# Optimization experiments

Hardware: AMD Instinct MI355X
Metric: run time of the kernel (lower is better)

The kernel has to match this reference:

```python
import jax, jax.numpy as jnp
import numpy as np

ATT_HEAD = 12
IN_DIM = 768
OUT_DIM = IN_DIM // ATT_HEAD
LEAKY_ALPHA = 0.2
B, N = 8, 512


def setup_inputs() -> dict:
    key = jax.random.key(0)
    ks = jax.random.split(key, 8)
    feat_in = jax.random.normal(ks[0], (B, N, IN_DIM), dtype=jnp.float32)
    adj = jax.random.randint(ks[1], (B, N, N), 0, 2) > 0
    # xavier_uniform for W: fan_in=in_dim, fan_out=out_dim
    lim_W = float(np.sqrt(6.0 / (IN_DIM + OUT_DIM)))
    W = jax.random.uniform(ks[2], (ATT_HEAD, IN_DIM, OUT_DIM), minval=-lim_W, maxval=lim_W, dtype=jnp.float32)
    b = jnp.zeros((OUT_DIM,), dtype=jnp.float32)
    lim_w = float(np.sqrt(6.0 / (OUT_DIM + 1)))
    w_src = jax.random.uniform(ks[3], (ATT_HEAD, OUT_DIM, 1), minval=-lim_w, maxval=lim_w, dtype=jnp.float32)
    w_dst = jax.random.uniform(ks[4], (ATT_HEAD, OUT_DIM, 1), minval=-lim_w, maxval=lim_w, dtype=jnp.float32)
    # xavier_normal for H.weight [in_dim, in_dim]
    std_H = float(np.sqrt(2.0 / (IN_DIM + IN_DIM)))
    H_w = jax.random.normal(ks[5], (IN_DIM, IN_DIM), dtype=jnp.float32) * std_H
    H_b = jax.random.normal(ks[6], (IN_DIM,), dtype=jnp.float32) * 0.01
    return {"feat_in": feat_in, "adj": adj, "W": W, "b": b,
            "w_src": w_src, "w_dst": w_dst, "H_w": H_w, "H_b": H_b}


def reference(feat_in, adj, W, b, w_src, w_dst, H_w, H_b):
    # h: [B, heads, N, out_dim]
    h = jnp.einsum('bnd,ade->bane', feat_in, W)
    th = jnp.tanh(h)
    attn_src = jnp.einsum('bane,aeo->bano', th, w_src)  # [B,A,N,1]
    attn_dst = jnp.einsum('bane,aeo->bano', th, w_dst)  # [B,A,N,1]
    attn = attn_src + jnp.swapaxes(attn_dst, 2, 3)      # [B,A,N,N]
    attn = jnp.where(attn >= 0, attn, LEAKY_ALPHA * attn)
    mask = ~adj[:, None, :, :]                           # [B,1,N,N]
    attn = jnp.where(mask, jnp.float32(-999.0), attn)
    attn = jax.nn.softmax(attn, axis=-1)
    feat_out = jnp.einsum('banm,bame->bane', attn, h) + b
    feat_out = jnp.swapaxes(feat_out, 1, 2).reshape(feat_in.shape[0], feat_in.shape[1], -1)
    feat_out = jax.nn.elu(feat_out)
    gate = jax.nn.sigmoid(feat_in @ H_w.T + H_b)
    return gate * feat_out + (1.0 - gate) * feat_in
```

## Files before the change

kernel.cpp:

```cpp
#include <hip/hip_runtime.h>
#include <hip/hip_bf16.h>

#define BB 8
#define NN 512
#define AH 12
#define DIN 768
#define EE 64
#define MM (BB*NN)
#define YY (BB*AH)
#define LEAKY 0.2f

typedef unsigned short u16;
typedef unsigned int u32;
typedef __attribute__((ext_vector_type(8))) short short8;
typedef __attribute__((ext_vector_type(4))) float f32x4;
typedef __attribute__((ext_vector_type(4))) u32 u32x4;

static __device__ __forceinline__ u16 f2bf(float f) {
    u32 u = __builtin_bit_cast(u32, f);
    u32 r = (u + 0x7FFFu + ((u >> 16) & 1u)) >> 16;
    return (u16)r;
}
static __device__ __forceinline__ u32 pk2(float a, float b) {
    return (u32)f2bf(a) | ((u32)f2bf(b) << 16);
}
static __device__ __forceinline__ u32 pk2t(float a, float b) {
    return (__builtin_bit_cast(u32, a) >> 16) | (__builtin_bit_cast(u32, b) & 0xFFFF0000u);
}
static __device__ __forceinline__ float ftanh(float x) {
    x = fminf(fmaxf(x, -15.f), 15.f);
    return 1.f - 2.f / (__expf(2.f * x) + 1.f);
}
static __device__ __forceinline__ float sigm(float z) {
    z = fminf(fmaxf(z, -80.f), 80.f);
    return 1.f / (1.f + __expf(-z));
}
static __device__ __forceinline__ void gl_lds16(const u16* g, u16* l) {
    __builtin_amdgcn_global_load_lds((const __attribute__((address_space(1))) unsigned int*)g,
                                     (__attribute__((address_space(3))) unsigned int*)l,
                                     16, 0, 0);
}

static __device__ __forceinline__ void mfma_probe(int lane, int* prow, int* pcol) {
    int q = lane >> 4, x = lane & 15;
    short8 af, bf;
#pragma unroll
    for (int j = 0; j < 8; j++) {
        int k = q * 8 + j;
        af[j] = (short)f2bf((k < 16) ? (float)(x * 16 + k) : 0.f);
        bf[j] = (short)f2bf((k == x) ? 1.f : 0.f);
    }
    f32x4 d = {};
    d = __builtin_amdgcn_mfma_f32_16x16x32_bf16(af, bf, d, 0, 0, 0);
#pragma unroll
    for (int r = 0; r < 4; r++) {
        int v = (int)(d[r] + 0.5f);
        prow[r] = v >> 4;
        pcol[r] = v & 15;
    }
}

#define N_FEAT (MM*DIN)
#define N_W    (AH*DIN*EE)
#define PACK_BLOCKS (MM/4)
#define CONV_BLOCKS ((N_FEAT + 2*N_W)/256)
__global__ __launch_bounds__(256) void prep_kernel(const int* __restrict__ adj,
                                                   const float* __restrict__ feat,
                                                   const float* __restrict__ W,
                                                   const float* __restrict__ Hw,
                                                   u32* __restrict__ maskbuf,
                                                   u16* __restrict__ featb,
                                                   u16* __restrict__ Wt,
                                                   u16* __restrict__ Hwb) {
    int blk = blockIdx.x, t = threadIdx.x;
    if (blk < PACK_BLOCKS) {
        int w = t >> 6, ln = t & 63;
        int row = blk * 4 + w;
        const int* ar = adj + (size_t)row * NN;
#pragma unroll
        for (int it = 0; it < 8; it++) {
            unsigned long long bal = __ballot(ar[it * 64 + ln] != 0);
            if (ln == 0) {
                maskbuf[row * 16 + it * 2]     = (u32)bal;
                maskbuf[row * 16 + it * 2 + 1] = (u32)(bal >> 32);
            }
        }
        return;
    }
    int i = (blk - PACK_BLOCKS) * 256 + t;
    if (i < N_FEAT) { featb[i] = f2bf(feat[i]); return; }
    int i2 = i - N_FEAT;
    if (i2 < N_W) {
        int a = i2 / (DIN * EE), rem = i2 % (DIN * EE);
        int e = rem / DIN, d = rem % DIN;
        Wt[i2] = f2bf(W[a * (DIN * EE) + d * EE + e]);
        return;
    }
    int i3 = i2 - N_W;
    Hwb[i3] = f2bf(Hw[i3]);
}

__global__ __launch_bounds__(256) void gemm_fused_kernel(const u16* __restrict__ featb,
                                                         const u16* __restrict__ Wt,
                                                         const u16* __restrict__ Hwb,
                                                         const float* __restrict__ wsrc,
                                                         const float* __restrict__ wdst,
                                                         const float* __restrict__ Hb,
                                                         u16* __restrict__ hT,
                                                         float2* __restrict__ Spair,
                                                         float2* __restrict__ Dpair,
                                                         float* __restrict__ Gbuf) {
    __shared__ u16 As[64 * 64];
    __shared__ u16 BsW[64 * 64];
    __shared__ u16 BsG[64 * 64];
    __shared__ alignas(16) float cs[64][68];
    int t = threadIdx.x, w = t >> 6, lane = t & 63, q = lane >> 4, x = lane & 15;
    int m0 = blockIdx.x * 64, a = blockIdx.y;

    int wm = w & 1, wn = w >> 1, xr = x & 7;
    int srow = t >> 3;
    int skoff = ((t & 7) ^ (srow & 7)) * 8;
    const u16* Agp  = featb + (size_t)m0 * DIN + srow * DIN + skoff;
    const u16* BWgp = Wt + (size_t)a * EE * DIN + srow * DIN + skoff;
    const u16* BGgp = Hwb + (size_t)(a * EE) * DIN + srow * DIN + skoff;
    u16* Asw  = As  + w * 512;
    u16* BWsw = BsW + w * 512;
    u16* BGsw = BsG + w * 512;
    const u16* ApA  = As  + (wm * 32 + x) * 64;
    const u16* ApBW = BsW + (wn * 32 + x) * 64;
    const u16* ApBG = BsG + (wn * 32 + x) * 64;
    f32x4 aW00 = {}, aW01 = {}, aW10 = {}, aW11 = {};
    f32x4 aG00 = {}, aG01 = {}, aG10 = {}, aG11 = {};

    for (int k0 = 0; k0 < DIN; k0 += 64) {
        gl_lds16(Agp + k0, Asw);
        gl_lds16(Agp + 32 * DIN + k0, Asw + 2048);
        gl_lds16(BWgp + k0, BWsw);
        gl_lds16(BWgp + 32 * DIN + k0, BWsw + 2048);
        gl_lds16(BGgp + k0, BGsw);
        gl_lds16(BGgp + 32 * DIN + k0, BGsw + 2048);
        __syncthreads();
#pragma unroll
        for (int kk = 0; kk < 2; kk++) {
            int c8 = ((q + kk * 4) ^ xr) * 8;
            short8 a0 = *(const short8*)(ApA + c8);
            short8 a1 = *(const short8*)(ApA + 16 * 64 + c8);
            short8 bW0 = *(const short8*)(ApBW + c8);
            short8 bW1 = *(const short8*)(ApBW + 16 * 64 + c8);
            short8 bG0 = *(const short8*)(ApBG + c8);
            short8 bG1 = *(const short8*)(ApBG + 16 * 64 + c8);
            aW00 = __builtin_amdgcn_mfma_f32_16x16x32_bf16(a0, bW0, aW00, 0, 0, 0);
            aW01 = __builtin_amdgcn_mfma_f32_16x16x32_bf16(a0, bW1, aW01, 0, 0, 0);
            aW10 = __builtin_amdgcn_mfma_f32_16x16x32_bf16(a1, bW0, aW10, 0, 0, 0);
            aW11 = __builtin_amdgcn_mfma_f32_16x16x32_bf16(a1, bW1, aW11, 0, 0, 0);
            aG00 = __builtin_amdgcn_mfma_f32_16x16x32_bf16(a0, bG0, aG00, 0, 0, 0);
            aG01 = __builtin_amdgcn_mfma_f32_16x16x32_bf16(a0, bG1, aG01, 0, 0, 0);
            aG10 = __builtin_amdgcn_mfma_f32_16x16x32_bf16(a1, bG0, aG10, 0, 0, 0);
            aG11 = __builtin_amdgcn_mfma_f32_16x16x32_bf16(a1, bG1, aG11, 0, 0, 0);
        }
        __syncthreads();
    }

    int prow[4], pcol[4];
    mfma_probe(lane, prow, pcol);

#pragma unroll
    for (int r = 0; r < 4; r++) {
        cs[wm * 32 + prow[r]][wn * 32 + pcol[r]]           = aW00[r];
        cs[wm * 32 + prow[r]][wn * 32 + 16 + pcol[r]]      = aW01[r];
        cs[wm * 32 + 16 + prow[r]][wn * 32 + pcol[r]]      = aW10[r];
        cs[wm * 32 + 16 + prow[r]][wn * 32 + 16 + pcol[r]] = aW11[r];
    }
    __syncthreads();

    int b = m0 >> 9;
    int y = b * AH + a;
    int nbase = m0 & 511;
    {
        int kcb = nbase >> 3;
#pragma unroll
        for (int i = 0; i < 2; i++) {
            int idx = i * 256 + t;
            int kcl = idx >> 6, e = idx & 63;
            int r0 = kcl * 8;
            u32x4 wv = { pk2(cs[r0 + 0][e], cs[r0 + 1][e]),
                         pk2(cs[r0 + 2][e], cs[r0 + 3][e]),
                         pk2(cs[r0 + 4][e], cs[r0 + 5][e]),
                         pk2(cs[r0 + 6][e], cs[r0 + 7][e]) };
            *(u32x4*)&hT[((((size_t)y << 6) + kcb + kcl) << 6 | e) * 8] = wv;
        }
    }
    {
        int r = t >> 2, cg = t & 3;
        float s = 0.f, d = 0.f;
#pragma unroll
        for (int i = 0; i < 16; i++) {
            int e2 = cg * 16 + i;
            float th = ftanh(cs[r][e2]);
            s += th * wsrc[a * EE + e2];
            d += th * wdst[a * EE + e2];
        }
        s += __shfl_xor(s, 1); s += __shfl_xor(s, 2);
        d += __shfl_xor(d, 1); d += __shfl_xor(d, 2);
        if (cg == 0) {
            s = fminf(fmaxf(s, -40.f), 40.f);
            d = fminf(fmaxf(d, -40.f), 40.f);
            Spair[y * NN + nbase + r] = make_float2(__expf(s), __expf(0.2f * s));
            Dpair[y * NN + nbase + r] = make_float2(__expf(d), __expf(0.2f * d));
        }
    }
    __syncthreads();

#pragma unroll
    for (int r = 0; r < 4; r++) {
        cs[wm * 32 + prow[r]][wn * 32 + pcol[r]]           = aG00[r];
        cs[wm * 32 + prow[r]][wn * 32 + 16 + pcol[r]]      = aG01[r];
        cs[wm * 32 + 16 + prow[r]][wn * 32 + pcol[r]]      = aG10[r];
        cs[wm * 32 + 16 + prow[r]][wn * 32 + 16 + pcol[r]] = aG11[r];
    }
    __syncthreads();

    {
        int n0 = a * EE;
        float4 hb = *(const float4*)&Hb[n0 + (t & 15) * 4];
#pragma unroll
        for (int p = 0; p < 4; p++) {
            int ml = p * 16 + (t >> 4), c4 = (t & 15) * 4;
            float4 v4 = *(const float4*)&cs[ml][c4];
            size_t idx = (size_t)(m0 + ml) * DIN + n0 + c4;
            float4 o;
            o.x = sigm(v4.x + hb.x);
            o.y = sigm(v4.y + hb.y);
            o.z = sigm(v4.z + hb.z);
            o.w = sigm(v4.w + hb.w);
            *(float4*)&Gbuf[idx] = o;
        }
    }
}

__global__ __launch_bounds__(256) void attn_kernel(const u16* __restrict__ hT,
                                                   const float2* __restrict__ Spair,
                                                   const float2* __restrict__ Dpair,
                                                   const u32* __restrict__ maskbuf,
                                                   const float* __restrict__ bias,
                                                   const float* __restrict__ Gbuf,
                                                   const float* __restrict__ feat,
                                                   float* __restrict__ out) {
    __shared__ alignas(16) float2 sd2[NN];
    __shared__ u32 smask[64][17];
    __shared__ float silv[64];
    __shared__ alignas(16) float cs[64][68];

    int t = threadIdx.x;
    int y = blockIdx.y, bb = y / AH, a = y % AH;
    int i0 = blockIdx.x * 64;
    int w = t >> 6, lane = t & 63, q = lane >> 4, x = lane & 15;

    sd2[t] = Dpair[y * NN + t];
    sd2[t + 256] = Dpair[y * NN + 256 + t];
#pragma unroll
    for (int p = 0; p < 4; p++) {
        int idx = p * 256 + t, r = idx >> 4, c = idx & 15;
        smask[r][c] = maskbuf[((bb << 9) + i0 + r) * 16 + c];
    }
    __syncthreads();

    int rowl = w * 16 + x;
    float2 se = Spair[y * NN + i0 + rowl];
    float es1 = se.x, es2 = se.y;

    u32 anym = 0;
#pragma unroll
    for (int c = 0; c < 16; c++) anym |= smask[rowl][c];
    int uni = (anym == 0);

    const u16* hTy = hT + ((size_t)y << 12) * 8;
    f32x4 acc[4] = {};
    float lsum = 0.f;

#pragma unroll 2
    for (int k0 = 0; k0 < NN; k0 += 32) {
        u32 mb = smask[rowl][k0 >> 5] >> (q * 8);
        float pv[8];
#pragma unroll
        for (int j = 0; j < 8; j++) {
            float2 dp = sd2[k0 + q * 8 + j];
            float m1 = es1 * dp.x;
            float m2 = es2 * dp.y;
            float p = (m1 >= 1.f) ? m1 : m2;
            p = ((mb >> j) & 1) ? p : 0.f;
            p = uni ? 1.0f : p;
            lsum += p;
            pv[j] = p;
        }
        short8 af = __builtin_bit_cast(short8, (u32x4){
            pk2t(pv[0], pv[1]), pk2t(pv[2], pv[3]),
            pk2t(pv[4], pv[5]), pk2t(pv[6], pv[7])});
        const u16* hp = hTy + ((((k0 >> 3) + q) << 6) + x) * 8;
        short8 b0 = *(const short8*)(hp);
        short8 b1 = *(const short8*)(hp + 16 * 8);
        short8 b2 = *(const short8*)(hp + 32 * 8);
        short8 b3 = *(const short8*)(hp + 48 * 8);
        acc[0] = __builtin_amdgcn_mfma_f32_16x16x32_bf16(af, b0, acc[0], 0, 0, 0);
        acc[1] = __builtin_amdgcn_mfma_f32_16x16x32_bf16(af, b1, acc[1], 0, 0, 0);
        acc[2] = __builtin_amdgcn_mfma_f32_16x16x32_bf16(af, b2, acc[2], 0, 0, 0);
        acc[3] = __builtin_amdgcn_mfma_f32_16x16x32_bf16(af, b3, acc[3], 0, 0, 0);
    }

    lsum += __shfl_xor(lsum, 16);
    lsum += __shfl_xor(lsum, 32);
    if (q == 0) silv[rowl] = 1.f / fmaxf(lsum, 1e-30f);

    int prow[4], pcol[4];
    mfma_probe(lane, prow, pcol);
#pragma unroll
    for (int nt = 0; nt < 4; nt++)
#pragma unroll
        for (int r = 0; r < 4; r++)
            cs[w * 16 + prow[r]][nt * 16 + pcol[r]] = acc[nt][r];
    __syncthreads();

    float4 b4 = *(const float4*)&bias[(t & 15) * 4];
#pragma unroll
    for (int p = 0; p < 4; p++) {
        int nl = p * 16 + (t >> 4), e4 = (t & 15) * 4;
        float il = silv[nl];
        float4 c4 = *(const float4*)&cs[nl][e4];
        size_t base = ((size_t)(bb << 9) + i0 + nl) * DIN + a * EE + e4;
        float4 g4 = *(const float4*)&Gbuf[base];
        float4 f4 = *(const float4*)&feat[base];
        float4 o;
        float v, e;
        v = c4.x * il + b4.x; e = v > 0.f ? v : __expf(v) - 1.f; o.x = g4.x * e + (1.f - g4.x) * f4.x;
        v = c4.y * il + b4.y; e = v > 0.f ? v : __expf(v) - 1.f; o.y = g4.y * e + (1.f - g4.y) * f4.y;
        v = c4.z * il + b4.z; e = v > 0.f ? v : __expf(v) - 1.f; o.z = g4.z * e + (1.f - g4.z) * f4.z;
        v = c4.w * il + b4.w; e = v > 0.f ? v : __expf(v) - 1.f; o.w = g4.w * e + (1.f - g4.w) * f4.w;
        *(float4*)&out[base] = o;
    }
}

extern "C" void kernel_launch(void* const* d_in, const int* in_sizes, int n_in,
                              void* d_out, int out_size, void* d_ws, size_t ws_size,
                              hipStream_t stream) {
    const float* feat  = (const float*)d_in[0];
    const int*   adj   = (const int*)  d_in[1];
    const float* W     = (const float*)d_in[2];
    const float* bvec  = (const float*)d_in[3];
    const float* wsrc  = (const float*)d_in[4];
    const float* wdst  = (const float*)d_in[5];
    const float* Hw    = (const float*)d_in[6];
    const float* Hb    = (const float*)d_in[7];
    float* out = (float*)d_out;

    char* ws = (char*)d_ws;
    u16*    featb   = (u16*)(ws);
    u16*    Wt      = (u16*)(ws + 6291456);
    u16*    Hwb     = (u16*)(ws + 7471104);
    u16*    hT      = (u16*)(ws + 8650752);
    float2* Spair   = (float2*)(ws + 14942208);
    float2* Dpair   = (float2*)(ws + 15335424);
    u32*    maskbuf = (u32*)(ws + 15728640);
    float*  Gbuf    = (float*)(ws + 15990784);

    prep_kernel<<<PACK_BLOCKS + CONV_BLOCKS, 256, 0, stream>>>(
        adj, feat, W, Hw, maskbuf, featb, Wt, Hwb);
    gemm_fused_kernel<<<dim3(MM / 64, AH), 256, 0, stream>>>(
        featb, Wt, Hwb, wsrc, wdst, Hb, hT, Spair, Dpair, Gbuf);
    attn_kernel<<<dim3(NN / 64, YY), 256, 0, stream>>>(
        hT, Spair, Dpair, maskbuf, bvec, Gbuf, feat, out);
}
```

Baseline: 122.4 us.

## Vectorize prep conversions, tile W transpose via LDS, streamline attention prob packing

The prep kernel now converts feat and H_w to bf16 four elements per thread with float4 loads, and transposes W through a shared-memory tile so both reads and writes are coalesced. Previously each of those elements was handled by its own thread, and the W transpose did strided global reads. In the attention loop, pairs of float2 loads become float4 loads, the compare-select becomes fmaxf, and truncating bf16 packing is replaced by the hardware v_cvt_pk_bf16_f32 instruction. That instruction rounds where the old code truncated, so the numerics shift slightly. Swapping the select for fmaxf assumes the two stored exponent products relate the way the original condition did.

Result: no change. 120.9 us (-1.3%).

```diff
diff --git a/kernel.cpp b/kernel.cpp
--- a/kernel.cpp
+++ b/kernel.cpp
@@ -15,6 +15,7 @@
 typedef __attribute__((ext_vector_type(8))) short short8;
 typedef __attribute__((ext_vector_type(4))) float f32x4;
 typedef __attribute__((ext_vector_type(4))) u32 u32x4;
+typedef __attribute__((ext_vector_type(4))) u16 u16x4;
 
 static __device__ __forceinline__ u16 f2bf(float f) {
     u32 u = __builtin_bit_cast(u32, f);
@@ -24,8 +25,10 @@
 static __device__ __forceinline__ u32 pk2(float a, float b) {
     return (u32)f2bf(a) | ((u32)f2bf(b) << 16);
 }
-static __device__ __forceinline__ u32 pk2t(float a, float b) {
-    return (__builtin_bit_cast(u32, a) >> 16) | (__builtin_bit_cast(u32, b) & 0xFFFF0000u);
+static __device__ __forceinline__ u32 cvtpk(float a, float b) {
+    u32 r;
+    asm("v_cvt_pk_bf16_f32 %0, %1, %2" : "=v"(r) : "v"(a), "v"(b));
+    return r;
 }
 static __device__ __forceinline__ float ftanh(float x) {
     x = fminf(fmaxf(x, -15.f), 15.f);
@@ -63,7 +66,11 @@
 #define N_FEAT (MM*DIN)
 #define N_W    (AH*DIN*EE)
 #define PACK_BLOCKS (MM/4)
-#define CONV_BLOCKS ((N_FEAT + 2*N_W)/256)
+#define FEATV_BLOCKS (N_FEAT/1024)
+#define HWBV_BLOCKS (N_W/1024)
+#define WT_BLOCKS (AH*(DIN/64))
+#define PREP_BLOCKS (PACK_BLOCKS + FEATV_BLOCKS + HWBV_BLOCKS + WT_BLOCKS)
+
 __global__ __launch_bounds__(256) void prep_kernel(const int* __restrict__ adj,
                                                    const float* __restrict__ feat,
                                                    const float* __restrict__ W,
@@ -87,17 +94,43 @@
         }
         return;
     }
-    int i = (blk - PACK_BLOCKS) * 256 + t;
-    if (i < N_FEAT) { featb[i] = f2bf(feat[i]); return; }
-    int i2 = i - N_FEAT;
-    if (i2 < N_W) {
-        int a = i2 / (DIN * EE), rem = i2 % (DIN * EE);
-        int e = rem / DIN, d = rem % DIN;
-        Wt[i2] = f2bf(W[a * (DIN * EE) + d * EE + e]);
+    blk -= PACK_BLOCKS;
+    if (blk < FEATV_BLOCKS) {
+        int i = blk * 1024 + t * 4;
+        float4 v = *(const float4*)&feat[i];
+        u16x4 o = { f2bf(v.x), f2bf(v.y), f2bf(v.z), f2bf(v.w) };
+        *(u16x4*)&featb[i] = o;
         return;
     }
-    int i3 = i2 - N_W;
-    Hwb[i3] = f2bf(Hw[i3]);
+    blk -= FEATV_BLOCKS;
+    if (blk < HWBV_BLOCKS) {
+        int i = blk * 1024 + t * 4;
+        float4 v = *(const float4*)&Hw[i];
+        u16x4 o = { f2bf(v.x), f2bf(v.y), f2bf(v.z), f2bf(v.w) };
+        *(u16x4*)&Hwb[i] = o;
+        return;
+    }
+    blk -= HWBV_BLOCKS;
+    __shared__ float tile[64][65];
+    int a = blk / (DIN / 64), d0 = (blk % (DIN / 64)) * 64;
+    int rl = t >> 4, c4 = (t & 15) * 4;
+#pragma unroll
+    for (int i = 0; i < 4; i++) {
+        int dl = i * 16 + rl;
+        float4 v = *(const float4*)&W[((size_t)a * DIN + d0 + dl) * EE + c4];
+        tile[dl][c4 + 0] = v.x;
+        tile[dl][c4 + 1] = v.y;
+        tile[dl][c4 + 2] = v.z;
+        tile[dl][c4 + 3] = v.w;
+    }
+    __syncthreads();
+#pragma unroll
+    for (int i = 0; i < 4; i++) {
+        int e = i * 16 + rl;
+        u16x4 o = { f2bf(tile[c4 + 0][e]), f2bf(tile[c4 + 1][e]),
+                    f2bf(tile[c4 + 2][e]), f2bf(tile[c4 + 3][e]) };
+        *(u16x4*)&Wt[(size_t)a * EE * DIN + (size_t)e * DIN + d0 + c4] = o;
+    }
 }
 
 __global__ __launch_bounds__(256) void gemm_fused_kernel(const u16* __restrict__ featb,
@@ -281,21 +314,24 @@
 #pragma unroll 2
     for (int k0 = 0; k0 < NN; k0 += 32) {
         u32 mb = smask[rowl][k0 >> 5] >> (q * 8);
+        const float4* sdp = (const float4*)&sd2[k0 + q * 8];
         float pv[8];
 #pragma unroll
-        for (int j = 0; j < 8; j++) {
-            float2 dp = sd2[k0 + q * 8 + j];
-            float m1 = es1 * dp.x;
-            float m2 = es2 * dp.y;
-            float p = (m1 >= 1.f) ? m1 : m2;
-            p = ((mb >> j) & 1) ? p : 0.f;
-            p = uni ? 1.0f : p;
-            lsum += p;
-            pv[j] = p;
+        for (int jj = 0; jj < 4; jj++) {
+            float4 d4 = sdp[jj];
+            float p0 = fmaxf(es1 * d4.x, es2 * d4.y);
+            float p1 = fmaxf(es1 * d4.z, es2 * d4.w);
+            p0 = ((mb >> (2 * jj)) & 1) ? p0 : 0.f;
+            p1 = ((mb >> (2 * jj + 1)) & 1) ? p1 : 0.f;
+            p0 = uni ? 1.0f : p0;
+            p1 = uni ? 1.0f : p1;
+            lsum += p0 + p1;
+            pv[2 * jj] = p0;
+            pv[2 * jj + 1] = p1;
         }
         short8 af = __builtin_bit_cast(short8, (u32x4){
-            pk2t(pv[0], pv[1]), pk2t(pv[2], pv[3]),
-            pk2t(pv[4], pv[5]), pk2t(pv[6], pv[7])});
+            cvtpk(pv[0], pv[1]), cvtpk(pv[2], pv[3]),
+            cvtpk(pv[4], pv[5]), cvtpk(pv[6], pv[7])});
         const u16* hp = hTy + ((((k0 >> 3) + q) << 6) + x) * 8;
         short8 b0 = *(const short8*)(hp);
         short8 b1 = *(const short8*)(hp + 16 * 8);
@@ -362,7 +398,7 @@
     u32*    maskbuf = (u32*)(ws + 15728640);
     float*  Gbuf    = (float*)(ws + 15990784);
 
-    prep_kernel<<<PACK_BLOCKS + CONV_BLOCKS, 256, 0, stream>>>(
+    prep_kernel<<<PREP_BLOCKS, 256, 0, stream>>>(
         adj, feat, W, Hw, maskbuf, featb, Wt, Hwb);
     gemm_fused_kernel<<<dim3(MM / 64, AH), 256, 0, stream>>>(
         featb, Wt, Hwb, wsrc, wdst, Hb, hT, Spair, Dpair, Gbuf);
```
